# Kernel optimization log

Measured on AMD Instinct MI355X. Metric: run time of the kernel, lower is better.

Reference implementation:

```python
import jax, jax.numpy as jnp
import numpy as np

B, T, H, D = 4, 2048, 16, 64
HID = H * D
ROPE_THETA = 10000.0


def _rope_tables(t, d, theta):
    # frequencies over half the head dim, duplicated to full head_dim
    inv_freq = 1.0 / (theta ** (np.arange(0, d, 2, dtype=np.float32) / d))  # (d/2,)
    pos = np.arange(t, dtype=np.float32)
    freqs = np.outer(pos, inv_freq)                      # (T, d/2)
    emb = np.concatenate([freqs, freqs], axis=-1)        # (T, d)
    return jnp.asarray(np.cos(emb)), jnp.asarray(np.sin(emb))


def setup_inputs() -> dict:
    key = jax.random.key(0)
    ks = jax.random.split(key, 5)
    s = 1.0 / np.sqrt(HID)
    cos, sin = _rope_tables(T, D, ROPE_THETA)
    return {
        "x": jax.random.normal(ks[0], (B, T, HID), dtype=jnp.float32),
        "cos": cos,
        "sin": sin,
        "wq": jax.random.normal(ks[1], (HID, HID), dtype=jnp.float32) * s,
        "wk": jax.random.normal(ks[2], (HID, HID), dtype=jnp.float32) * s,
        "wv": jax.random.normal(ks[3], (HID, HID), dtype=jnp.float32) * s,
        "wo": jax.random.normal(ks[4], (HID, HID), dtype=jnp.float32) * s,
    }


def _rotate_half(x):
    x1, x2 = jnp.split(x, 2, axis=-1)
    return jnp.concatenate([-x2, x1], axis=-1)


def reference(x, cos, sin, wq, wk, wv, wo):
    b, t, _ = x.shape
    # QKV projections (nn.Linear: y = x @ W^T), reshape to (B, H, T, D)
    q = (x @ wq.T).reshape(b, t, H, D).transpose(0, 2, 1, 3)
    k = (x @ wk.T).reshape(b, t, H, D).transpose(0, 2, 1, 3)
    v = (x @ wv.T).reshape(b, t, H, D).transpose(0, 2, 1, 3)
    # RoPE
    c = cos[None, None, :, :]
    s = sin[None, None, :, :]
    q = q * c + _rotate_half(q) * s
    k = k * c + _rotate_half(k) * s
    # causal SDPA
    scale = 1.0 / jnp.sqrt(jnp.asarray(D, dtype=x.dtype))
    scores = jnp.einsum("bhqd,bhkd->bhqk", q, k) * scale
    causal = jnp.tril(jnp.ones((t, t), dtype=bool))
    scores = jnp.where(causal[None, None], scores, jnp.finfo(scores.dtype).min)
    attn = jax.nn.softmax(scores, axis=-1)
    out = jnp.einsum("bhqk,bhkd->bhqd", attn, v)
    out = out.transpose(0, 2, 1, 3).reshape(b, t, HID)
    return out @ wo.T
```

## Files before the change

### kernel.cpp

```cpp
#include <hip/hip_runtime.h>

#define BSZ 4
#define TT 2048
#define NH 16
#define HD 64
#define HID 1024
#define BT 8192
#define BH 64

typedef unsigned short u16;
typedef unsigned int u32;
typedef unsigned long long u64;
typedef __attribute__((ext_vector_type(4))) float f32x4;
typedef __attribute__((ext_vector_type(8))) short bf16x8;

#define MFMA32(a, b, c) __builtin_amdgcn_mfma_f32_16x16x32_bf16(a, b, c, 0, 0, 0)

typedef const __attribute__((address_space(1))) u32* gp32;
typedef __attribute__((address_space(3))) u32* lp32;

__device__ __forceinline__ u16 f2bf(float f) {
    union { float f; u32 u; } x; x.f = f;
    u32 r = x.u + 0x7FFFu + ((x.u >> 16) & 1u);
    return (u16)(r >> 16);
}

__global__ __launch_bounds__(256) void cast_kernel(const float* __restrict__ src,
                                                   u16* __restrict__ dst, int n4) {
    int i = blockIdx.x * 256 + threadIdx.x;
    if (i >= n4) return;
    f32x4 v = *(const f32x4*)(src + (size_t)i * 4);
    uint2 u;
    u.x = (u32)f2bf(v[0]) | ((u32)f2bf(v[1]) << 16);
    u.y = (u32)f2bf(v[2]) | ((u32)f2bf(v[3]) << 16);
    *(uint2*)(dst + (size_t)i * 4) = u;
}

template<int MODE>
__global__ __launch_bounds__(512, 2)
void gemm_bt(const u16* __restrict__ A, const u16* __restrict__ W,
             float* __restrict__ Cf, u16* __restrict__ qkv, u16* __restrict__ vt,
             const float* __restrict__ cosT, const float* __restrict__ sinT) {
    __shared__ __align__(16) u16 sh[3 * 24576];
    const int tid  = threadIdx.x;
    const int wid  = tid >> 6, lane = tid & 63;
    const int lrow = lane & 15, lk = lane >> 4;
    const int wm   = (wid >> 1) * 64, wn = (wid & 1) * 64;
    const int m0   = blockIdx.x * 256, n0 = blockIdx.y * 128;

    auto stageA = [&](int buf, int kk, int half) {
        u16* dst = sh + buf * 24576;
        #pragma unroll
        for (int s = 0; s < 2; ++s) {
            int l16 = half * 1024 + s * 512 + tid;
            int r = l16 >> 3, c = l16 & 7;
            int gc = (c ^ (r & 7)) * 8;
            __builtin_amdgcn_global_load_lds(
                (gp32)&A[(size_t)(m0 + r) * HID + kk + gc],
                (lp32)&dst[l16 * 8], 16, 0, 0);
        }
    };
    auto stageB = [&](int buf, int kk) {
        u16* dst = sh + buf * 24576 + 16384;
        #pragma unroll
        for (int s = 0; s < 2; ++s) {
            int l16 = s * 512 + tid;
            int r = l16 >> 3, c = l16 & 7;
            int gc = (c ^ (r & 7)) * 8;
            __builtin_amdgcn_global_load_lds(
                (gp32)&W[(size_t)(n0 + r) * HID + kk + gc],
                (lp32)&dst[l16 * 8], 16, 0, 0);
        }
    };

    f32x4 acc[4][4] = {};

    stageA(0, 0, 0); stageA(0, 0, 1); stageB(0, 0);
    stageA(1, 64, 0); stageA(1, 64, 1); stageB(1, 64);

    int b = 0;
    for (int t = 0; t < 16; ++t) {
        if (t < 15) asm volatile("s_waitcnt vmcnt(6)" ::: "memory");
        else        asm volatile("s_waitcnt vmcnt(0)" ::: "memory");
        __builtin_amdgcn_s_barrier();
        const u16* As = sh + b * 24576;
        const u16* Bs = As + 16384;
        int b2 = b + 2; if (b2 >= 3) b2 -= 3;
        const bool st  = (t + 2 < 16);
        const int kk2  = (t + 2) * 64;

        #pragma unroll
        for (int h = 0; h < 2; ++h) {
            bf16x8 af[4], bfr[4];
            #pragma unroll
            for (int i = 0; i < 4; ++i) {
                int row = wm + i * 16 + lrow;
                int pc  = (h * 4 + lk) ^ (row & 7);
                af[i] = *(const bf16x8*)&As[row * 64 + pc * 8];
            }
            #pragma unroll
            for (int j = 0; j < 4; ++j) {
                int row = wn + j * 16 + lrow;
                int pc  = (h * 4 + lk) ^ (row & 7);
                bfr[j] = *(const bf16x8*)&Bs[row * 64 + pc * 8];
            }
            if (st) {
                if (h == 0) { stageA(b2, kk2, 0); stageB(b2, kk2); }
                else        { stageA(b2, kk2, 1); }
            }
            __builtin_amdgcn_s_barrier();
            asm volatile("s_waitcnt lgkmcnt(0)" ::: "memory");
            __builtin_amdgcn_sched_barrier(0);
            __builtin_amdgcn_s_setprio(1);
            #pragma unroll
            for (int i = 0; i < 4; ++i)
                #pragma unroll
                for (int j = 0; j < 4; ++j)
                    acc[i][j] = MFMA32(af[i], bfr[j], acc[i][j]);
            __builtin_amdgcn_s_setprio(0);
            __builtin_amdgcn_sched_barrier(0);
            __builtin_amdgcn_s_barrier();
        }
        ++b; if (b == 3) b = 0;
    }
    __syncthreads();

    if (MODE == 0) {
        const int bb = m0 >> 11, tl0 = m0 & (TT - 1);
        if (blockIdx.y < 16) {
            const float QSC = (blockIdx.y < 8) ? 0.125f * 1.44269504f : 1.0f;
            #pragma unroll
            for (int i = 0; i < 4; ++i)
                #pragma unroll
                for (int r = 0; r < 4; ++r) {
                    int tl = (m0 + wm + i * 16 + lk * 4 + r) & (TT - 1);
                    #pragma unroll
                    for (int j = 0; j < 2; ++j) {
                        int dd = j * 16 + lrow;
                        float c = cosT[tl * HD + dd], s = sinT[tl * HD + dd];
                        float v1 = acc[i][j][r], v2 = acc[i][j + 2][r];
                        acc[i][j][r]     = (v1 * c - v2 * s) * QSC;
                        acc[i][j + 2][r] = (v2 * c + v1 * s) * QSC;
                    }
                }
            #pragma unroll
            for (int i = 0; i < 4; ++i)
                #pragma unroll
                for (int j = 0; j < 4; ++j)
                    #pragma unroll
                    for (int r = 0; r < 4; ++r)
                        sh[(wm + i * 16 + lk * 4 + r) * 136 + wn + j * 16 + lrow] =
                            f2bf(acc[i][j][r]);
            __syncthreads();
            #pragma unroll
            for (int p = 0; p < 8; ++p) {
                int idx = p * 512 + tid;
                int r = idx >> 4, c16 = idx & 15;
                f32x4 v = *(const f32x4*)&sh[r * 136 + c16 * 8];
                int nfull = n0 + c16 * 8;
                int proj = nfull >> 10, nl = nfull & 1023;
                int h = nl >> 6, d = nl & 63;
                u16* dst = qkv + (size_t)proj * BT * HID +
                           (((size_t)(bb * NH + h) * TT + tl0 + r) * HD + d);
                *(f32x4*)dst = v;
            }
        } else {
            #pragma unroll
            for (int i = 0; i < 4; ++i)
                #pragma unroll
                for (int j = 0; j < 4; ++j)
                    #pragma unroll
                    for (int r = 0; r < 4; ++r)
                        sh[(wn + j * 16 + lrow) * 272 + wm + i * 16 + lk * 4 + r] =
                            f2bf(acc[i][j][r]);
            __syncthreads();
            #pragma unroll
            for (int p = 0; p < 8; ++p) {
                int oc  = p * 512 + tid;
                int t8  = oc & 31;
                int col = oc >> 5;
                f32x4 v = *(const f32x4*)&sh[col * 272 + t8 * 8];
                int nl = (n0 - 2048) + col;
                int h = nl >> 6, d = nl & 63;
                *(f32x4*)&vt[((size_t)(bb * NH + h) * HD + d) * TT + tl0 + t8 * 8] = v;
            }
        }
    } else {
        #pragma unroll
        for (int i = 0; i < 4; ++i)
            #pragma unroll
            for (int j = 0; j < 4; ++j)
                #pragma unroll
                for (int r = 0; r < 4; ++r) {
                    int m = m0 + wm + i * 16 + lk * 4 + r;
                    int n = n0 + wn + j * 16 + lrow;
                    Cf[(size_t)m * HID + n] = acc[i][j][r];
                }
    }
}

__device__ __forceinline__ u32 cvtpk(float lo, float hi) {
    u32 r;
    asm("v_cvt_pk_bf16_f32 %0, %1, %2" : "=v"(r) : "v"(lo), "v"(hi));
    return r;
}
__device__ __forceinline__ bf16x8 packP(const f32x4& a, const f32x4& b) {
    union { bf16x8 v; u32 w[4]; } u;
    u.w[0] = cvtpk(a[0], a[1]); u.w[1] = cvtpk(a[2], a[3]);
    u.w[2] = cvtpk(b[0], b[1]); u.w[3] = cvtpk(b[2], b[3]);
    return u.v;
}

#define VST 68

__global__ __launch_bounds__(256)
void attn_kernel(const u16* __restrict__ q, const u16* __restrict__ k,
                 const u16* __restrict__ vt, u16* __restrict__ o) {
    __shared__ u16 Ks[64 * 72];
    __shared__ u16 Vts[64 * VST];
    const int tid  = threadIdx.x;
    const int w    = tid >> 6, lane = tid & 63;
    const int lrow = lane & 15, lk = lane >> 4;
    const int nlid = (blockIdx.x & 7) * 128 + (blockIdx.x >> 3);
    const int p    = nlid & 15;
    const int bh   = nlid >> 4;
    const int q0a  = 64 * p, q0b = 64 * (31 - p);
    const size_t hb = (size_t)bh * TT * HD;

    bf16x8 qfa[2], qfb[2];
    #pragma unroll
    for (int kq = 0; kq < 2; ++kq) {
        qfa[kq] = *(const bf16x8*)&q[hb + (size_t)(q0a + w * 16 + lrow) * HD + kq * 32 + lk * 8];
        qfb[kq] = *(const bf16x8*)&q[hb + (size_t)(q0b + w * 16 + lrow) * HD + kq * 32 + lk * 8];
    }

    f32x4 oa[4] = {}, obc[4] = {};
    float lia = 0.f, lib = 0.f;

    const int r0 = tid >> 3, f0 = (tid & 7) * 8;
    const int r1 = (tid + 256) >> 3, f1 = (tid & 7) * 8;

    f32x4 pk0 = *(const f32x4*)&k[hb + (size_t)r0 * HD + f0];
    f32x4 pk1 = *(const f32x4*)&k[hb + (size_t)r1 * HD + f1];
    f32x4 pv0 = *(const f32x4*)&vt[hb + (size_t)r0 * TT + f0];
    f32x4 pv1 = *(const f32x4*)&vt[hb + (size_t)r1 * TT + f1];

    const int nIter = 32 - p;
    for (int it = 0; it < nIter; ++it) {
        const bool a_act = (it <= p);
        __syncthreads();
        *(f32x4*)&Ks[r0 * 72 + f0]   = pk0;
        *(f32x4*)&Ks[r1 * 72 + f1]   = pk1;
        *(f32x4*)&Vts[r0 * VST + f0] = pv0;
        *(f32x4*)&Vts[r1 * VST + f1] = pv1;
        __syncthreads();
        if (it + 1 < nIter) {
            const int nn = (it + 1) * 64;
            pk0 = *(const f32x4*)&k[hb + (size_t)(nn + r0) * HD + f0];
            pk1 = *(const f32x4*)&k[hb + (size_t)(nn + r1) * HD + f1];
            pv0 = *(const f32x4*)&vt[hb + (size_t)r0 * TT + nn + f0];
            pv1 = *(const f32x4*)&vt[hb + (size_t)r1 * TT + nn + f1];
        }

        bf16x8 kf0[4], kf1[4];
        #pragma unroll
        for (int mt = 0; mt < 4; ++mt) {
            kf0[mt] = *(const bf16x8*)&Ks[(mt * 16 + lrow) * 72 + lk * 8];
            kf1[mt] = *(const bf16x8*)&Ks[(mt * 16 + lrow) * 72 + 32 + lk * 8];
        }

        {
            f32x4 s[4] = {};
            __builtin_amdgcn_s_setprio(1);
            #pragma unroll
            for (int mt = 0; mt < 4; ++mt) {
                s[mt] = MFMA32(kf0[mt], qfb[0], s[mt]);
                s[mt] = MFMA32(kf1[mt], qfb[1], s[mt]);
            }
            __builtin_amdgcn_s_setprio(0);
            if (it == nIter - 1) {
                #pragma unroll
                for (int mt = 0; mt < 4; ++mt)
                    #pragma unroll
                    for (int r = 0; r < 4; ++r)
                        if (mt * 16 + lk * 4 + r > w * 16 + lrow) s[mt][r] = -1e30f;
            }
            #pragma unroll
            for (int mt = 0; mt < 4; ++mt)
                #pragma unroll
                for (int r = 0; r < 4; ++r) {
                    float pv = exp2f(s[mt][r]);
                    s[mt][r] = pv; lib += pv;
                }
            bf16x8 p0 = packP(s[0], s[1]), p1 = packP(s[2], s[3]);
            __builtin_amdgcn_s_setprio(1);
            #pragma unroll
            for (int t2 = 0; t2 < 2; ++t2)
                #pragma unroll
                for (int dm = 0; dm < 4; ++dm) {
                    union { bf16x8 v; struct { u64 lo, hi; } u; } vf;
                    const u16* vrow = &Vts[(dm * 16 + lrow) * VST + t2 * 32 + lk * 4];
                    vf.u.lo = *(const u64*)vrow;
                    vf.u.hi = *(const u64*)(vrow + 16);
                    obc[dm] = MFMA32(vf.v, t2 ? p1 : p0, obc[dm]);
                }
            __builtin_amdgcn_s_setprio(0);
        }

        if (a_act) {
            f32x4 s[4] = {};
            __builtin_amdgcn_s_setprio(1);
            #pragma unroll
            for (int mt = 0; mt < 4; ++mt) {
                s[mt] = MFMA32(kf0[mt], qfa[0], s[mt]);
                s[mt] = MFMA32(kf1[mt], qfa[1], s[mt]);
            }
            __builtin_amdgcn_s_setprio(0);
            if (it == p) {
                #pragma unroll
                for (int mt = 0; mt < 4; ++mt)
                    #pragma unroll
                    for (int r = 0; r < 4; ++r)
                        if (mt * 16 + lk * 4 + r > w * 16 + lrow) s[mt][r] = -1e30f;
            }
            #pragma unroll
            for (int mt = 0; mt < 4; ++mt)
                #pragma unroll
                for (int r = 0; r < 4; ++r) {
                    float pv = exp2f(s[mt][r]);
                    s[mt][r] = pv; lia += pv;
                }
            bf16x8 p0 = packP(s[0], s[1]), p1 = packP(s[2], s[3]);
            __builtin_amdgcn_s_setprio(1);
            #pragma unroll
            for (int t2 = 0; t2 < 2; ++t2)
                #pragma unroll
                for (int dm = 0; dm < 4; ++dm) {
                    union { bf16x8 v; struct { u64 lo, hi; } u; } vf;
                    const u16* vrow = &Vts[(dm * 16 + lrow) * VST + t2 * 32 + lk * 4];
                    vf.u.lo = *(const u64*)vrow;
                    vf.u.hi = *(const u64*)(vrow + 16);
                    oa[dm] = MFMA32(vf.v, t2 ? p1 : p0, oa[dm]);
                }
            __builtin_amdgcn_s_setprio(0);
        }
    }

    lia += __shfl_xor(lia, 16, 64); lia += __shfl_xor(lia, 32, 64);
    lib += __shfl_xor(lib, 16, 64); lib += __shfl_xor(lib, 32, 64);
    const int b = bh >> 4, h = bh & 15;
    const float inva = 1.f / lia, invb = 1.f / lib;
    #pragma unroll
    for (int dm = 0; dm < 4; ++dm) {
        uint2 pk;
        pk.x = cvtpk(oa[dm][0] * inva, oa[dm][1] * inva);
        pk.y = cvtpk(oa[dm][2] * inva, oa[dm][3] * inva);
        int row = q0a + w * 16 + lrow;
        *(uint2*)&o[((size_t)(b * TT + row)) * HID + h * HD + dm * 16 + lk * 4] = pk;
        pk.x = cvtpk(obc[dm][0] * invb, obc[dm][1] * invb);
        pk.y = cvtpk(obc[dm][2] * invb, obc[dm][3] * invb);
        row = q0b + w * 16 + lrow;
        *(uint2*)&o[((size_t)(b * TT + row)) * HID + h * HD + dm * 16 + lk * 4] = pk;
    }
}

extern "C" void kernel_launch(void* const* d_in, const int* in_sizes, int n_in,
                              void* d_out, int out_size, void* d_ws, size_t ws_size,
                              hipStream_t stream) {
    const float* x    = (const float*)d_in[0];
    const float* cosT = (const float*)d_in[1];
    const float* sinT = (const float*)d_in[2];
    const float* wq   = (const float*)d_in[3];
    const float* wk   = (const float*)d_in[4];
    const float* wv   = (const float*)d_in[5];
    const float* wo   = (const float*)d_in[6];
    float* out = (float*)d_out;

    char* ws = (char*)d_ws;
    size_t off = 0;
    u16* x_bf  = (u16*)(ws + off); off += (size_t)BT * HID * 2;
    u16* wqkv  = (u16*)(ws + off); off += (size_t)3 * HID * HID * 2;
    u16* wo_bf = (u16*)(ws + off); off += (size_t)HID * HID * 2;
    u16* qb    = (u16*)(ws + off); off += (size_t)BT * HID * 2;
    u16* kb    = (u16*)(ws + off); off += (size_t)BT * HID * 2;
    u16* vtb   = (u16*)(ws + off); off += (size_t)BT * HID * 2;
    u16* ob    = (u16*)(ws + off); off += (size_t)BT * HID * 2;
    (void)kb;

    cast_kernel<<<(BT * HID / 4 + 255) / 256, 256, 0, stream>>>(x, x_bf, BT * HID / 4);
    cast_kernel<<<1024, 256, 0, stream>>>(wq, wqkv, HID * HID / 4);
    cast_kernel<<<1024, 256, 0, stream>>>(wk, wqkv + (size_t)HID * HID, HID * HID / 4);
    cast_kernel<<<1024, 256, 0, stream>>>(wv, wqkv + (size_t)2 * HID * HID, HID * HID / 4);
    cast_kernel<<<1024, 256, 0, stream>>>(wo, wo_bf, HID * HID / 4);

    gemm_bt<0><<<dim3(BT / 256, 3 * HID / 128), 512, 0, stream>>>(
        x_bf, wqkv, nullptr, qb, vtb, cosT, sinT);

    attn_kernel<<<dim3(1024), 256, 0, stream>>>(qb, kb, vtb, ob);

    gemm_bt<1><<<dim3(BT / 256, HID / 128), 512, 0, stream>>>(
        ob, wo_bf, out, nullptr, nullptr, nullptr, nullptr);
}
```

Baseline: 266.8 us.

## Fuse weight casts, remap GEMM tiles per XCD, and use raw exp2 in attention

Merges the four weight-cast launches into one kernel. Switches both GEMMs to a 1D grid whose block index is remapped so that consecutive tiles stay on the same XCD, which should improve L2 reuse. In attention, it replaces exp2f with an inline v_exp_f32 and accumulates the row sums as vectors to shorten the serial add chains. Together these aim to cut launch overhead, cache misses and ALU latency. The raw exp skips exp2f's range handling, which slightly changes numerics for extreme inputs.

```diff
diff --git a/kernel.cpp b/kernel.cpp
--- a/kernel.cpp
+++ b/kernel.cpp
@@ -25,10 +25,31 @@
     return (u16)(r >> 16);
 }
 
+__device__ __forceinline__ float fexp2(float x) {
+    float r;
+    asm("v_exp_f32 %0, %1\n\ts_nop 1" : "=v"(r) : "v"(x));
+    return r;
+}
+
 __global__ __launch_bounds__(256) void cast_kernel(const float* __restrict__ src,
                                                    u16* __restrict__ dst, int n4) {
     int i = blockIdx.x * 256 + threadIdx.x;
     if (i >= n4) return;
+    f32x4 v = *(const f32x4*)(src + (size_t)i * 4);
+    uint2 u;
+    u.x = (u32)f2bf(v[0]) | ((u32)f2bf(v[1]) << 16);
+    u.y = (u32)f2bf(v[2]) | ((u32)f2bf(v[3]) << 16);
+    *(uint2*)(dst + (size_t)i * 4) = u;
+}
+
+__global__ __launch_bounds__(256)
+void cast_w_kernel(const float* __restrict__ wq, const float* __restrict__ wk,
+                   const float* __restrict__ wv, const float* __restrict__ wo,
+                   u16* __restrict__ wqkv, u16* __restrict__ wo_bf) {
+    int g = blockIdx.x >> 10;
+    int i = (blockIdx.x & 1023) * 256 + threadIdx.x;
+    const float* src = (g == 0) ? wq : (g == 1) ? wk : (g == 2) ? wv : wo;
+    u16* dst = (g == 3) ? wo_bf : wqkv + (size_t)g * HID * HID;
     f32x4 v = *(const f32x4*)(src + (size_t)i * 4);
     uint2 u;
     u.x = (u32)f2bf(v[0]) | ((u32)f2bf(v[1]) << 16);
@@ -46,7 +67,10 @@
     const int wid  = tid >> 6, lane = tid & 63;
     const int lrow = lane & 15, lk = lane >> 4;
     const int wm   = (wid >> 1) * 64, wn = (wid & 1) * 64;
-    const int m0   = blockIdx.x * 256, n0 = blockIdx.y * 128;
+    const int NT   = (MODE == 0) ? 96 : 32;
+    const int nlid = (blockIdx.x & 7) * NT + (blockIdx.x >> 3);
+    const int mt   = nlid & 31, nt = nlid >> 5;
+    const int m0   = mt * 256, n0 = nt * 128;
 
     auto stageA = [&](int buf, int kk, int half) {
         u16* dst = sh + buf * 24576;
@@ -127,8 +151,8 @@
 
     if (MODE == 0) {
         const int bb = m0 >> 11, tl0 = m0 & (TT - 1);
-        if (blockIdx.y < 16) {
-            const float QSC = (blockIdx.y < 8) ? 0.125f * 1.44269504f : 1.0f;
+        if (nt < 16) {
+            const float QSC = (nt < 8) ? 0.125f * 1.44269504f : 1.0f;
             #pragma unroll
             for (int i = 0; i < 4; ++i)
                 #pragma unroll
@@ -235,7 +259,7 @@
     }
 
     f32x4 oa[4] = {}, obc[4] = {};
-    float lia = 0.f, lib = 0.f;
+    f32x4 la4 = {}, lb4 = {};
 
     const int r0 = tid >> 3, f0 = (tid & 7) * 8;
     const int r1 = (tid + 256) >> 3, f1 = (tid & 7) * 8;
@@ -286,12 +310,11 @@
                         if (mt * 16 + lk * 4 + r > w * 16 + lrow) s[mt][r] = -1e30f;
             }
             #pragma unroll
-            for (int mt = 0; mt < 4; ++mt)
-                #pragma unroll
-                for (int r = 0; r < 4; ++r) {
-                    float pv = exp2f(s[mt][r]);
-                    s[mt][r] = pv; lib += pv;
-                }
+            for (int mt = 0; mt < 4; ++mt) {
+                #pragma unroll
+                for (int r = 0; r < 4; ++r) s[mt][r] = fexp2(s[mt][r]);
+                lb4 += s[mt];
+            }
             bf16x8 p0 = packP(s[0], s[1]), p1 = packP(s[2], s[3]);
             __builtin_amdgcn_s_setprio(1);
             #pragma unroll
@@ -324,12 +347,11 @@
                         if (mt * 16 + lk * 4 + r > w * 16 + lrow) s[mt][r] = -1e30f;
             }
             #pragma unroll
-            for (int mt = 0; mt < 4; ++mt)
-                #pragma unroll
-                for (int r = 0; r < 4; ++r) {
-                    float pv = exp2f(s[mt][r]);
-                    s[mt][r] = pv; lia += pv;
-                }
+            for (int mt = 0; mt < 4; ++mt) {
+                #pragma unroll
+                for (int r = 0; r < 4; ++r) s[mt][r] = fexp2(s[mt][r]);
+                la4 += s[mt];
+            }
             bf16x8 p0 = packP(s[0], s[1]), p1 = packP(s[2], s[3]);
             __builtin_amdgcn_s_setprio(1);
             #pragma unroll
@@ -346,6 +368,8 @@
         }
     }
 
+    float lia = la4[0] + la4[1] + la4[2] + la4[3];
+    float lib = lb4[0] + lb4[1] + lb4[2] + lb4[3];
     lia += __shfl_xor(lia, 16, 64); lia += __shfl_xor(lia, 32, 64);
     lib += __shfl_xor(lib, 16, 64); lib += __shfl_xor(lib, 32, 64);
     const int b = bh >> 4, h = bh & 15;
@@ -388,16 +412,13 @@
     (void)kb;
 
     cast_kernel<<<(BT * HID / 4 + 255) / 256, 256, 0, stream>>>(x, x_bf, BT * HID / 4);
-    cast_kernel<<<1024, 256, 0, stream>>>(wq, wqkv, HID * HID / 4);
-    cast_kernel<<<1024, 256, 0, stream>>>(wk, wqkv + (size_t)HID * HID, HID * HID / 4);
-    cast_kernel<<<1024, 256, 0, stream>>>(wv, wqkv + (size_t)2 * HID * HID, HID * HID / 4);
-    cast_kernel<<<1024, 256, 0, stream>>>(wo, wo_bf, HID * HID / 4);
-
-    gemm_bt<0><<<dim3(BT / 256, 3 * HID / 128), 512, 0, stream>>>(
+    cast_w_kernel<<<4096, 256, 0, stream>>>(wq, wk, wv, wo, wqkv, wo_bf);
+
+    gemm_bt<0><<<dim3(768), 512, 0, stream>>>(
         x_bf, wqkv, nullptr, qb, vtb, cosT, sinT);
 
     attn_kernel<<<dim3(1024), 256, 0, stream>>>(qb, kb, vtb, ob);
 
-    gemm_bt<1><<<dim3(BT / 256, HID / 128), 512, 0, stream>>>(
+    gemm_bt<1><<<dim3(256), 512, 0, stream>>>(
         ob, wo_bf, out, nullptr, nullptr, nullptr, nullptr);
 }
```

New measurement: 267.9 us. About the same (+0.4%).
